# Kernel optimization log

Measured on AMD Instinct MI355X. Metric: run time of the kernel, lower is better.

Reference implementation:

```python
import jax, jax.numpy as jnp
import numpy as np

N, E, F, H = 100000, 1600000, 512, 256


def setup_inputs() -> dict:
    key = jax.random.key(0)
    ks = jax.random.split(key, 8)
    feat = jax.random.normal(ks[0], (N, F), dtype=jnp.float32)
    src = jax.random.randint(ks[1], (E,), 0, N, dtype=jnp.int32)
    dst = jax.random.randint(ks[2], (E,), 0, N, dtype=jnp.int32)
    W1 = jax.random.normal(ks[3], (F, H), dtype=jnp.float32) * 0.05
    b1 = jnp.zeros((H,), jnp.float32)
    W2 = jax.random.normal(ks[4], (H, H), dtype=jnp.float32) * 0.05
    b2 = jnp.zeros((H,), jnp.float32)
    Wg = jax.random.normal(ks[5], (3 * H, 2 * F), dtype=jnp.float32) * 0.05
    bg = jnp.zeros((2 * F,), jnp.float32)
    eps = jax.random.normal(ks[6], (F,), dtype=jnp.float32)
    return {"feat": feat, "src": src, "dst": dst, "node_index": 1234,
            "W1": W1, "b1": b1, "W2": W2, "b2": b2, "Wg": Wg, "bg": bg, "eps": eps}


def reference(feat, src, dst, node_index, W1, b1, W2, b2, Wg, bg, eps):
    n = feat.shape[0]
    ones_e = jnp.ones(src.shape[0], feat.dtype)
    out_deg = jax.ops.segment_sum(ones_e, src, num_segments=n)
    in_deg = jax.ops.segment_sum(ones_e, dst, num_segments=n)
    # DGL GraphConv(norm='both') clamps degrees to >= 1
    norm_src = jnp.maximum(out_deg, 1.0) ** -0.5  # [N]
    norm_dst = jnp.maximum(in_deg, 1.0) ** -0.5   # [N]

    def gconv(x, W, b):
        x = (x * norm_src[:, None]) @ W                      # weight first
        agg = jax.ops.segment_sum(x[src], dst, num_segments=n)  # sparse aggregate
        return agg * norm_dst[:, None] + b

    h = jax.nn.leaky_relu(gconv(feat, W1, b1), 0.01)
    h = jax.nn.leaky_relu(gconv(h, W2, b2), 0.01)
    pooled = jnp.concatenate([h.sum(0), h.max(0), h[node_index]])  # [3H]
    fd = pooled @ Wg + bg                                          # [2F]
    in_feats = feat.shape[1]
    mu = fd[:in_feats]
    sigma = jnp.abs(fd[in_feats:])
    # Normal.sample() is non-differentiable -> stop_gradient
    feat_new = jax.lax.stop_gradient(mu + sigma * eps)
    log2pi = jnp.float32(np.log(2.0 * np.pi))
    log_prob = jnp.mean(-0.5 * ((feat_new - mu) / sigma) ** 2 - jnp.log(sigma) - 0.5 * log2pi)
    return feat_new, mu, sigma, log_prob
```

## Files before the change

kernel.cpp:

```cpp
#include <hip/hip_runtime.h>
#include <math.h>

#define F_DIM 512
#define H_DIM 256

using v8bf  = __attribute__((ext_vector_type(8))) __bf16;
using f32x4 = __attribute__((ext_vector_type(4))) float;

__device__ __forceinline__ float bf2f(unsigned short u) {
    return __uint_as_float(((unsigned int)u) << 16);
}
__device__ __forceinline__ unsigned short f2bf(float f) {
    unsigned int x = __float_as_uint(f);
    unsigned int r = x + 0x7FFFu + ((x >> 16) & 1u);
    return (unsigned short)(r >> 16);
}
__device__ __forceinline__ float fp8_dec(unsigned b) {
    unsigned em = b & 0x7Fu;
    float v = (em >= 8u) ? __uint_as_float((em + 960u) << 20)
                         : (float)em * 0.001953125f;
    return (b & 0x80u) ? -v : v;
}
__device__ __forceinline__ unsigned fp8_enc(float f) {
    unsigned bits = __float_as_uint(f);
    unsigned s = (bits >> 31) << 7;
    unsigned r = bits + 0x7FFFFu + ((bits >> 20) & 1u);
    int e = (int)((r >> 23) & 0xFF);
    unsigned em;
    if (e >= 121) em = (unsigned)(((e - 120) << 3) | ((r >> 20) & 7u));
    else          em = (unsigned)__float2int_rn(fabsf(f) * 512.0f);
    return s | em;
}

__global__ void hist_kernel(const int* __restrict__ src, const int* __restrict__ dst,
                            int E, int* degO, int* degI) {
    int stride = gridDim.x * blockDim.x;
    for (int e = blockIdx.x * blockDim.x + threadIdx.x; e < E; e += stride) {
        atomicAdd(&degO[src[e]], 1);
        atomicAdd(&degI[dst[e]], 1);
    }
}

__global__ void norm_kernel(const int* __restrict__ degO, const int* __restrict__ degI,
                            int n, float* nsrc, float* ndst) {
    int i = blockIdx.x * blockDim.x + threadIdx.x;
    if (i < n) {
        nsrc[i] = rsqrtf(fmaxf((float)degO[i], 1.0f));
        ndst[i] = rsqrtf(fmaxf((float)degI[i], 1.0f));
    }
}

__global__ void scan1_kernel(const int* __restrict__ deg, int n, int* blocksums) {
    __shared__ int sm[256];
    int b = blockIdx.x, t = threadIdx.x;
    int base = b * 1024 + t * 4;
    int s = 0;
#pragma unroll
    for (int i = 0; i < 4; i++) { int idx = base + i; if (idx < n) s += deg[idx]; }
    sm[t] = s; __syncthreads();
    for (int off = 128; off > 0; off >>= 1) {
        if (t < off) sm[t] += sm[t + off];
        __syncthreads();
    }
    if (t == 0) blocksums[b] = sm[0];
}

__global__ void scan2_kernel(const int* __restrict__ blocksums, int nb, int* blockoffs) {
    if (threadIdx.x == 0 && blockIdx.x == 0) {
        int run = 0;
        for (int i = 0; i < nb; i++) { blockoffs[i] = run; run += blocksums[i]; }
    }
}

__global__ void scan3_kernel(const int* __restrict__ deg, int n,
                             const int* __restrict__ blockoffs, int* row_start) {
    __shared__ int sm[256];
    int b = blockIdx.x, t = threadIdx.x;
    int base = b * 1024 + t * 4;
    int v[4]; int s = 0;
#pragma unroll
    for (int i = 0; i < 4; i++) {
        int idx = base + i;
        v[i] = (idx < n) ? deg[idx] : 0;
        s += v[i];
    }
    sm[t] = s; __syncthreads();
    for (int off = 1; off < 256; off <<= 1) {
        int x = sm[t];
        int y = (t >= off) ? sm[t - off] : 0;
        __syncthreads();
        sm[t] = x + y;
        __syncthreads();
    }
    int run = blockoffs[b] + sm[t] - s;
#pragma unroll
    for (int i = 0; i < 4; i++) {
        int idx = base + i;
        if (idx < n) row_start[idx] = run;
        run += v[i];
    }
}

__global__ void csr_fill_kernel(const int* __restrict__ src, const int* __restrict__ dst,
                                int E, const int* __restrict__ row_start,
                                int* cursor, int* esrc) {
    int stride = gridDim.x * blockDim.x;
    for (int e = blockIdx.x * blockDim.x + threadIdx.x; e < E; e += stride) {
        int d = dst[e];
        int pos = atomicAdd(&cursor[d], 1);
        esrc[row_start[d] + pos] = src[e];
    }
}

__global__ void wt_kernel(const float* __restrict__ W, unsigned short* __restrict__ Wt, int K) {
    int idx = blockIdx.x * 256 + threadIdx.x;
    if (idx < 256 * K) {
        int n = idx / K, k = idx - n * K;
        Wt[idx] = f2bf(W[(size_t)k * 256 + n]);
    }
}

template<int KDIM, bool A_FP32>
__global__ __launch_bounds__(256) void gemm_mfma_kernel(
    const void* __restrict__ Aptr, const float* __restrict__ scale,
    const unsigned short* __restrict__ Wt, unsigned char* __restrict__ Xout, int M) {
    __shared__ unsigned short As[64 * 40];
    __shared__ unsigned short Bs[256 * 40];

    const int tid = threadIdx.x;
    const int wv = tid >> 6, ln = tid & 63;
    const int m0 = blockIdx.x * 64;
    const int sr = tid >> 2;
    const int sc = tid & 3;

    f32x4 acc[4][4];
#pragma unroll
    for (int i = 0; i < 4; i++)
#pragma unroll
        for (int j = 0; j < 4; j++) acc[i][j] = (f32x4){0.f, 0.f, 0.f, 0.f};

    const int gr = m0 + sr;
    const bool rok = (gr < M);
    float ns = 0.0f;
    if (A_FP32 && rok) ns = scale[gr];

    for (int k0 = 0; k0 < KDIM; k0 += 32) {
        if (A_FP32) {
            const float* A = (const float*)Aptr;
            float4 va = make_float4(0, 0, 0, 0), vb = make_float4(0, 0, 0, 0);
            if (rok) {
                const float* p = A + (size_t)gr * KDIM + k0 + sc * 8;
                va = *(const float4*)p;
                vb = *(const float4*)(p + 4);
            }
            uint4 u;
            u.x = (unsigned)f2bf(va.x * ns) | ((unsigned)f2bf(va.y * ns) << 16);
            u.y = (unsigned)f2bf(va.z * ns) | ((unsigned)f2bf(va.w * ns) << 16);
            u.z = (unsigned)f2bf(vb.x * ns) | ((unsigned)f2bf(vb.y * ns) << 16);
            u.w = (unsigned)f2bf(vb.z * ns) | ((unsigned)f2bf(vb.w * ns) << 16);
            *(uint4*)&As[sr * 40 + sc * 8] = u;
        } else {
            const unsigned short* A = (const unsigned short*)Aptr;
            uint4 u = make_uint4(0, 0, 0, 0);
            if (rok) u = *(const uint4*)(A + (size_t)gr * KDIM + k0 + sc * 8);
            *(uint4*)&As[sr * 40 + sc * 8] = u;
        }
#pragma unroll
        for (int i = 0; i < 4; i++) {
            int idx = tid + i * 256;
            int n = idx >> 2, ck = idx & 3;
            uint4 w = *(const uint4*)(Wt + (size_t)n * KDIM + k0 + ck * 8);
            *(uint4*)&Bs[n * 40 + ck * 8] = w;
        }
        __syncthreads();
        const int fr = ln & 15;
        const int kg = (ln >> 4) * 8;
        v8bf af[4], bfr[4];
#pragma unroll
        for (int mr = 0; mr < 4; mr++)
            af[mr] = *(const v8bf*)&As[(mr * 16 + fr) * 40 + kg];
#pragma unroll
        for (int nr = 0; nr < 4; nr++)
            bfr[nr] = *(const v8bf*)&Bs[(wv * 64 + nr * 16 + fr) * 40 + kg];
#pragma unroll
        for (int mr = 0; mr < 4; mr++)
#pragma unroll
            for (int nr = 0; nr < 4; nr++)
                acc[mr][nr] = __builtin_amdgcn_mfma_f32_16x16x32_bf16(
                    bfr[nr], af[mr], acc[mr][nr], 0, 0, 0);
        __syncthreads();
    }
#pragma unroll
    for (int mr = 0; mr < 4; mr++) {
        int grow = m0 + mr * 16 + (ln & 15);
        if (grow < M) {
#pragma unroll
            for (int nr = 0; nr < 4; nr++) {
                unsigned u = fp8_enc(acc[mr][nr][0]) | (fp8_enc(acc[mr][nr][1]) << 8) |
                             (fp8_enc(acc[mr][nr][2]) << 16) | (fp8_enc(acc[mr][nr][3]) << 24);
                *(unsigned*)(Xout + (size_t)grow * 256 + wv * 64 + nr * 16 + (ln >> 4) * 4) = u;
            }
        }
    }
}

__global__ __launch_bounds__(256) void agg_fp8_kernel(
    const unsigned char* __restrict__ xb, const int* __restrict__ esrc,
    const int* __restrict__ row_start, const int* __restrict__ degI,
    const float* __restrict__ norm_dst, const float* __restrict__ post_scale,
    const float* __restrict__ bias, unsigned short* __restrict__ hout, int n) {
    int wave = threadIdx.x >> 6;
    int lane = threadIdx.x & 63;
    int node = blockIdx.x * 4 + wave;
    if (node >= n) return;
    int start = row_start[node];
    int cnt = degI[node];

    float a0 = 0.f, a1 = 0.f, a2 = 0.f, a3 = 0.f;
    int j = 0;
    for (; j + 4 <= cnt; j += 4) {
        int s0 = esrc[start + j + 0];
        int s1 = esrc[start + j + 1];
        int s2 = esrc[start + j + 2];
        int s3 = esrc[start + j + 3];
        unsigned v0 = *(const unsigned*)(xb + (size_t)s0 * 256 + lane * 4);
        unsigned v1 = *(const unsigned*)(xb + (size_t)s1 * 256 + lane * 4);
        unsigned v2 = *(const unsigned*)(xb + (size_t)s2 * 256 + lane * 4);
        unsigned v3 = *(const unsigned*)(xb + (size_t)s3 * 256 + lane * 4);
        a0 += fp8_dec(v0 & 255u) + fp8_dec(v1 & 255u) + fp8_dec(v2 & 255u) + fp8_dec(v3 & 255u);
        a1 += fp8_dec((v0 >> 8) & 255u) + fp8_dec((v1 >> 8) & 255u) + fp8_dec((v2 >> 8) & 255u) + fp8_dec((v3 >> 8) & 255u);
        a2 += fp8_dec((v0 >> 16) & 255u) + fp8_dec((v1 >> 16) & 255u) + fp8_dec((v2 >> 16) & 255u) + fp8_dec((v3 >> 16) & 255u);
        a3 += fp8_dec(v0 >> 24) + fp8_dec(v1 >> 24) + fp8_dec(v2 >> 24) + fp8_dec(v3 >> 24);
    }
    for (; j < cnt; j++) {
        int s = esrc[start + j];
        unsigned v = *(const unsigned*)(xb + (size_t)s * 256 + lane * 4);
        a0 += fp8_dec(v & 255u);
        a1 += fp8_dec((v >> 8) & 255u);
        a2 += fp8_dec((v >> 16) & 255u);
        a3 += fp8_dec(v >> 24);
    }
    float nd = norm_dst[node];
    float ps = post_scale ? post_scale[node] : 1.0f;
    float4 bv = *(const float4*)(bias + lane * 4);
    float r0 = a0 * nd + bv.x;
    float r1 = a1 * nd + bv.y;
    float r2 = a2 * nd + bv.z;
    float r3 = a3 * nd + bv.w;
    r0 = ((r0 >= 0.f) ? r0 : 0.01f * r0) * ps;
    r1 = ((r1 >= 0.f) ? r1 : 0.01f * r1) * ps;
    r2 = ((r2 >= 0.f) ? r2 : 0.01f * r2) * ps;
    r3 = ((r3 >= 0.f) ? r3 : 0.01f * r3) * ps;
    ushort4 o;
    o.x = f2bf(r0); o.y = f2bf(r1); o.z = f2bf(r2); o.w = f2bf(r3);
    *(ushort4*)(hout + (size_t)node * 256 + lane * 4) = o;
}

__global__ void pool_partial_kernel(const unsigned short* __restrict__ h, int n,
                                    float* psum, float* pmax) {
    int b = blockIdx.x, t = threadIdx.x;
    int r0 = b * 128;
    int r1 = min(r0 + 128, n);
    float s = 0.0f, m = -INFINITY;
    for (int r = r0; r < r1; r++) {
        float v = bf2f(h[(size_t)r * 256 + t]);
        s += v;
        m = fmaxf(m, v);
    }
    psum[(size_t)b * 256 + t] = s;
    pmax[(size_t)b * 256 + t] = m;
}

__global__ void pool_mid_kernel(const float* __restrict__ psum, const float* __restrict__ pmax,
                                int nchunks, float* psum2, float* pmax2) {
    int b = blockIdx.x;
    int t = threadIdx.x;
    float s = 0.0f, m = -INFINITY;
    for (int c = b; c < nchunks; c += 32) {
        s += psum[(size_t)c * 256 + t];
        m = fmaxf(m, pmax[(size_t)c * 256 + t]);
    }
    psum2[(size_t)b * 256 + t] = s;
    pmax2[(size_t)b * 256 + t] = m;
}

__global__ void pool_final_kernel(const float* __restrict__ psum2, const float* __restrict__ pmax2,
                                  const unsigned short* __restrict__ h,
                                  const int* __restrict__ node_index, float* pooled) {
    int t = threadIdx.x;
    float s = 0.0f, m = -INFINITY;
#pragma unroll
    for (int c = 0; c < 32; c++) {
        s += psum2[(size_t)c * 256 + t];
        m = fmaxf(m, pmax2[(size_t)c * 256 + t]);
    }
    pooled[t] = s;
    pooled[256 + t] = m;
    pooled[512 + t] = bf2f(h[(size_t)(*node_index) * 256 + t]);
}

__global__ void head_gemm_kernel(const float* __restrict__ pooled,
                                 const float* __restrict__ Wg, float* fdp) {
    __shared__ float p[96];
    int t = threadIdx.x;
    int cb = blockIdx.x;
    int kb = blockIdx.y;
    if (t < 96) p[t] = pooled[kb * 96 + t];
    __syncthreads();
    int j = cb * 128 + t;
    float s = 0.0f;
#pragma unroll 8
    for (int i = 0; i < 96; i++) s += p[i] * Wg[(size_t)(kb * 96 + i) * 1024 + j];
    fdp[(size_t)kb * 1024 + j] = s;
}

__global__ void head_final_kernel(const float* __restrict__ fdp, const float* __restrict__ bg,
                                  const float* __restrict__ eps, float* __restrict__ out) {
    __shared__ float red[512];
    int t = threadIdx.x;
    float mu = bg[t];
    float sgr = bg[512 + t];
#pragma unroll
    for (int kb = 0; kb < 8; kb++) {
        mu  += fdp[(size_t)kb * 1024 + t];
        sgr += fdp[(size_t)kb * 1024 + 512 + t];
    }
    float sg = fabsf(sgr);
    float fn = mu + sg * eps[t];
    out[t] = fn;
    out[512 + t] = mu;
    out[1024 + t] = sg;
    float z = (fn - mu) / sg;
    const float LOG2PI = 1.8378770664093453f;
    float lp = -0.5f * z * z - logf(sg) - 0.5f * LOG2PI;
    red[t] = lp;
    __syncthreads();
    for (int off = 256; off > 0; off >>= 1) {
        if (t < off) red[t] += red[t + off];
        __syncthreads();
    }
    if (t == 0) out[1536] = red[0] / 512.0f;
}

extern "C" void kernel_launch(void* const* d_in, const int* in_sizes, int n_in,
                              void* d_out, int out_size, void* d_ws, size_t ws_size,
                              hipStream_t stream) {
    const float* feat = (const float*)d_in[0];
    const int* src    = (const int*)d_in[1];
    const int* dst    = (const int*)d_in[2];
    const int* nodeix = (const int*)d_in[3];
    const float* W1   = (const float*)d_in[4];
    const float* b1   = (const float*)d_in[5];
    const float* W2   = (const float*)d_in[6];
    const float* b2   = (const float*)d_in[7];
    const float* Wg   = (const float*)d_in[8];
    const float* bg   = (const float*)d_in[9];
    const float* eps  = (const float*)d_in[10];
    float* out = (float*)d_out;

    const int N = in_sizes[0] / F_DIM;
    const int E = in_sizes[1];

    char* ws = (char*)d_ws;
    size_t off = 0;
    auto alloc = [&](size_t bytes) -> char* {
        char* p = ws + off;
        off += (bytes + 511) & ~(size_t)511;
        return p;
    };
    int* degO      = (int*)alloc((size_t)N * 4);
    int* degI      = (int*)alloc((size_t)N * 4);
    float* nsrc    = (float*)alloc((size_t)N * 4);
    float* ndst    = (float*)alloc((size_t)N * 4);
    int* row_start = (int*)alloc((size_t)N * 4);
    int* cursor    = (int*)alloc((size_t)N * 4);
    int* blocksums = (int*)alloc(1024);
    int* blockoffs = (int*)alloc(1024);
    int* esrc      = (int*)alloc((size_t)E * 4);
    unsigned short* Wt1 = (unsigned short*)alloc((size_t)256 * F_DIM * 2);
    unsigned short* Wt2 = (unsigned short*)alloc((size_t)256 * H_DIM * 2);
    unsigned char* xbuf = (unsigned char*)alloc((size_t)N * H_DIM);
    unsigned short* hs  = (unsigned short*)alloc((size_t)N * H_DIM * 2);
    int nchunks = (N + 127) / 128;
    float* psum    = (float*)alloc((size_t)nchunks * 256 * 4);
    float* pmax    = (float*)alloc((size_t)nchunks * 256 * 4);
    float* psum2   = (float*)alloc((size_t)32 * 256 * 4);
    float* pmax2   = (float*)alloc((size_t)32 * 256 * 4);
    float* pooled  = (float*)alloc(768 * 4);
    float* fdp     = (float*)alloc((size_t)8 * 1024 * 4);

    hipMemsetAsync(degO, 0, (size_t)N * 4, stream);
    hipMemsetAsync(degI, 0, (size_t)N * 4, stream);
    hipMemsetAsync(cursor, 0, (size_t)N * 4, stream);

    hist_kernel<<<2048, 256, 0, stream>>>(src, dst, E, degO, degI);
    norm_kernel<<<(N + 255) / 256, 256, 0, stream>>>(degO, degI, N, nsrc, ndst);
    int nb = (N + 1023) / 1024;
    scan1_kernel<<<nb, 256, 0, stream>>>(degI, N, blocksums);
    scan2_kernel<<<1, 1, 0, stream>>>(blocksums, nb, blockoffs);
    scan3_kernel<<<nb, 256, 0, stream>>>(degI, N, blockoffs, row_start);
    csr_fill_kernel<<<2048, 256, 0, stream>>>(src, dst, E, row_start, cursor, esrc);

    wt_kernel<<<(256 * F_DIM + 255) / 256, 256, 0, stream>>>(W1, Wt1, F_DIM);
    wt_kernel<<<(256 * H_DIM + 255) / 256, 256, 0, stream>>>(W2, Wt2, H_DIM);

    int mblocks = (N + 63) / 64;
    gemm_mfma_kernel<F_DIM, true><<<mblocks, 256, 0, stream>>>(feat, nsrc, Wt1, xbuf, N);
    agg_fp8_kernel<<<(N + 3) / 4, 256, 0, stream>>>(xbuf, esrc, row_start, degI, ndst, nsrc, b1, hs, N);
    gemm_mfma_kernel<H_DIM, false><<<mblocks, 256, 0, stream>>>(hs, nullptr, Wt2, xbuf, N);
    agg_fp8_kernel<<<(N + 3) / 4, 256, 0, stream>>>(xbuf, esrc, row_start, degI, ndst, nullptr, b2, hs, N);
    pool_partial_kernel<<<nchunks, 256, 0, stream>>>(hs, N, psum, pmax);
    pool_mid_kernel<<<32, 256, 0, stream>>>(psum, pmax, nchunks, psum2, pmax2);
    pool_final_kernel<<<1, 256, 0, stream>>>(psum2, pmax2, hs, nodeix, pooled);
    head_gemm_kernel<<<dim3(8, 8), 128, 0, stream>>>(pooled, Wg, fdp);
    head_final_kernel<<<1, 512, 0, stream>>>(fdp, bg, eps, out);
}
```

Baseline: 924.8 us.

## Build CSR via two-level bucket partition with shared-memory atomics

Replaces the global-atomic degree histogram, three-kernel scan and atomic CSR fill with a bucketed counting sort. Edges are first partitioned into 512-node buckets using block-local shared counters, then each bucket builds its own degrees, row offsets and sorted edge list in shared memory. This targets the cost of scattered global atomics on node-level counters. In exchange it adds two E-sized scratch arrays and an extra pass over the edges, and it relies on node ids fitting in 17 bits and at most 200 buckets.

```diff
diff --git a/kernel.cpp b/kernel.cpp
--- a/kernel.cpp
+++ b/kernel.cpp
@@ -3,6 +3,8 @@
 
 #define F_DIM 512
 #define H_DIM 256
+#define NPB 512
+#define NBMAX 200
 
 using v8bf  = __attribute__((ext_vector_type(8))) __bf16;
 using f32x4 = __attribute__((ext_vector_type(4))) float;
@@ -32,12 +34,123 @@
     return s | em;
 }
 
-__global__ void hist_kernel(const int* __restrict__ src, const int* __restrict__ dst,
-                            int E, int* degO, int* degI) {
+__global__ __launch_bounds__(256) void bucket_count_kernel(
+    const int* __restrict__ src, const int* __restrict__ dst, int E, int nb,
+    int* bcntS, int* bcntD) {
+    __shared__ int cs[NBMAX], cd[NBMAX];
+    for (int i = threadIdx.x; i < nb; i += 256) { cs[i] = 0; cd[i] = 0; }
+    __syncthreads();
     int stride = gridDim.x * blockDim.x;
     for (int e = blockIdx.x * blockDim.x + threadIdx.x; e < E; e += stride) {
-        atomicAdd(&degO[src[e]], 1);
-        atomicAdd(&degI[dst[e]], 1);
+        atomicAdd(&cs[src[e] >> 9], 1);
+        atomicAdd(&cd[dst[e] >> 9], 1);
+    }
+    __syncthreads();
+    for (int i = threadIdx.x; i < nb; i += 256) {
+        if (cs[i]) atomicAdd(&bcntS[i], cs[i]);
+        if (cd[i]) atomicAdd(&bcntD[i], cd[i]);
+    }
+}
+
+__global__ void bucket_scan_kernel(const int* __restrict__ bcntS, const int* __restrict__ bcntD,
+                                   int nb, int* bbaseS, int* bbaseD, int* bcurS, int* bcurD) {
+    __shared__ int s1[256], s2[256];
+    int t = threadIdx.x;
+    int v1 = (t < nb) ? bcntS[t] : 0;
+    int v2 = (t < nb) ? bcntD[t] : 0;
+    s1[t] = v1; s2[t] = v2;
+    __syncthreads();
+    for (int off = 1; off < 256; off <<= 1) {
+        int a = s1[t], b = s2[t];
+        int a2 = (t >= off) ? s1[t - off] : 0;
+        int b2 = (t >= off) ? s2[t - off] : 0;
+        __syncthreads();
+        s1[t] = a + a2; s2[t] = b + b2;
+        __syncthreads();
+    }
+    if (t < nb) {
+        int eS = s1[t] - v1;
+        int eD = s2[t] - v2;
+        bbaseS[t] = eS; bbaseD[t] = eD;
+        bcurS[t] = eS;  bcurD[t] = eD;
+    }
+}
+
+__global__ __launch_bounds__(256) void partition_kernel(
+    const int* __restrict__ src, const int* __restrict__ dst, int E, int chunk, int nb,
+    int* bcurS, int* bcurD, int* __restrict__ psrc, unsigned* __restrict__ pdst) {
+    __shared__ int cs[NBMAX], cd[NBMAX], ws[NBMAX], wd[NBMAX];
+    int t = threadIdx.x;
+    for (int i = t; i < nb; i += 256) { cs[i] = 0; cd[i] = 0; }
+    __syncthreads();
+    int e0 = blockIdx.x * chunk, e1 = min(e0 + chunk, E);
+    for (int e = e0 + t; e < e1; e += 256) {
+        atomicAdd(&cs[src[e] >> 9], 1);
+        atomicAdd(&cd[dst[e] >> 9], 1);
+    }
+    __syncthreads();
+    for (int i = t; i < nb; i += 256) {
+        ws[i] = cs[i] ? atomicAdd(&bcurS[i], cs[i]) : 0;
+        wd[i] = cd[i] ? atomicAdd(&bcurD[i], cd[i]) : 0;
+    }
+    __syncthreads();
+    for (int e = e0 + t; e < e1; e += 256) {
+        int s = src[e], d = dst[e];
+        int pS = atomicAdd(&ws[s >> 9], 1);
+        psrc[pS] = s;
+        int pD = atomicAdd(&wd[d >> 9], 1);
+        pdst[pD] = (unsigned)s | ((unsigned)(d & (NPB - 1)) << 17);
+    }
+}
+
+__global__ __launch_bounds__(256) void bucket_csr_kernel(
+    const unsigned* __restrict__ pdst, const int* __restrict__ psrc,
+    const int* __restrict__ bbaseS, const int* __restrict__ bcntS,
+    const int* __restrict__ bbaseD, const int* __restrict__ bcntD,
+    int* __restrict__ degO, int* __restrict__ degI,
+    int* __restrict__ row_start, int* __restrict__ esrc, int n) {
+    __shared__ int deg[NPB];
+    __shared__ int cur[NPB];
+    __shared__ int ps[256];
+    int b = blockIdx.x, t = threadIdx.x;
+    int nbase = b << 9;
+    for (int i = t; i < NPB; i += 256) deg[i] = 0;
+    __syncthreads();
+    int eb = bbaseD[b], ec = bcntD[b];
+    for (int i = t; i < ec; i += 256) atomicAdd(&deg[pdst[eb + i] >> 17], 1);
+    __syncthreads();
+    int d0 = deg[2 * t], d1 = deg[2 * t + 1];
+    ps[t] = d0 + d1;
+    __syncthreads();
+    for (int off = 1; off < 256; off <<= 1) {
+        int v = ps[t];
+        int u = (t >= off) ? ps[t - off] : 0;
+        __syncthreads();
+        ps[t] = v + u;
+        __syncthreads();
+    }
+    int ep = ps[t] - (d0 + d1);
+    int n0 = nbase + 2 * t, n1 = nbase + 2 * t + 1;
+    if (n0 < n) { degI[n0] = d0; row_start[n0] = eb + ep; }
+    if (n1 < n) { degI[n1] = d1; row_start[n1] = eb + ep + d0; }
+    cur[2 * t] = ep;
+    cur[2 * t + 1] = ep + d0;
+    __syncthreads();
+    for (int i = t; i < ec; i += 256) {
+        unsigned v = pdst[eb + i];
+        int l = v >> 17;
+        int p = atomicAdd(&cur[l], 1);
+        esrc[eb + p] = (int)(v & 0x1FFFFu);
+    }
+    __syncthreads();
+    for (int i = t; i < NPB; i += 256) deg[i] = 0;
+    __syncthreads();
+    int sb = bbaseS[b], sc = bcntS[b];
+    for (int i = t; i < sc; i += 256) atomicAdd(&deg[psrc[sb + i] & (NPB - 1)], 1);
+    __syncthreads();
+    for (int i = t; i < NPB; i += 256) {
+        int g = nbase + i;
+        if (g < n) degO[g] = deg[i];
     }
 }
 
@@ -47,68 +160,6 @@
     if (i < n) {
         nsrc[i] = rsqrtf(fmaxf((float)degO[i], 1.0f));
         ndst[i] = rsqrtf(fmaxf((float)degI[i], 1.0f));
-    }
-}
-
-__global__ void scan1_kernel(const int* __restrict__ deg, int n, int* blocksums) {
-    __shared__ int sm[256];
-    int b = blockIdx.x, t = threadIdx.x;
-    int base = b * 1024 + t * 4;
-    int s = 0;
-#pragma unroll
-    for (int i = 0; i < 4; i++) { int idx = base + i; if (idx < n) s += deg[idx]; }
-    sm[t] = s; __syncthreads();
-    for (int off = 128; off > 0; off >>= 1) {
-        if (t < off) sm[t] += sm[t + off];
-        __syncthreads();
-    }
-    if (t == 0) blocksums[b] = sm[0];
-}
-
-__global__ void scan2_kernel(const int* __restrict__ blocksums, int nb, int* blockoffs) {
-    if (threadIdx.x == 0 && blockIdx.x == 0) {
-        int run = 0;
-        for (int i = 0; i < nb; i++) { blockoffs[i] = run; run += blocksums[i]; }
-    }
-}
-
-__global__ void scan3_kernel(const int* __restrict__ deg, int n,
-                             const int* __restrict__ blockoffs, int* row_start) {
-    __shared__ int sm[256];
-    int b = blockIdx.x, t = threadIdx.x;
-    int base = b * 1024 + t * 4;
-    int v[4]; int s = 0;
-#pragma unroll
-    for (int i = 0; i < 4; i++) {
-        int idx = base + i;
-        v[i] = (idx < n) ? deg[idx] : 0;
-        s += v[i];
-    }
-    sm[t] = s; __syncthreads();
-    for (int off = 1; off < 256; off <<= 1) {
-        int x = sm[t];
-        int y = (t >= off) ? sm[t - off] : 0;
-        __syncthreads();
-        sm[t] = x + y;
-        __syncthreads();
-    }
-    int run = blockoffs[b] + sm[t] - s;
-#pragma unroll
-    for (int i = 0; i < 4; i++) {
-        int idx = base + i;
-        if (idx < n) row_start[idx] = run;
-        run += v[i];
-    }
-}
-
-__global__ void csr_fill_kernel(const int* __restrict__ src, const int* __restrict__ dst,
-                                int E, const int* __restrict__ row_start,
-                                int* cursor, int* esrc) {
-    int stride = gridDim.x * blockDim.x;
-    for (int e = blockIdx.x * blockDim.x + threadIdx.x; e < E; e += stride) {
-        int d = dst[e];
-        int pos = atomicAdd(&cursor[d], 1);
-        esrc[row_start[d] + pos] = src[e];
     }
 }
 
@@ -360,6 +411,7 @@
 
     const int N = in_sizes[0] / F_DIM;
     const int E = in_sizes[1];
+    const int nb = (N + NPB - 1) / NPB;
 
     char* ws = (char*)d_ws;
     size_t off = 0;
@@ -373,9 +425,14 @@
     float* nsrc    = (float*)alloc((size_t)N * 4);
     float* ndst    = (float*)alloc((size_t)N * 4);
     int* row_start = (int*)alloc((size_t)N * 4);
-    int* cursor    = (int*)alloc((size_t)N * 4);
-    int* blocksums = (int*)alloc(1024);
-    int* blockoffs = (int*)alloc(1024);
+    int* bcntS     = (int*)alloc(NBMAX * 4);
+    int* bcntD     = (int*)alloc(NBMAX * 4);
+    int* bbaseS    = (int*)alloc(NBMAX * 4);
+    int* bbaseD    = (int*)alloc(NBMAX * 4);
+    int* bcurS     = (int*)alloc(NBMAX * 4);
+    int* bcurD     = (int*)alloc(NBMAX * 4);
+    int* psrc      = (int*)alloc((size_t)E * 4);
+    unsigned* pdst = (unsigned*)alloc((size_t)E * 4);
     int* esrc      = (int*)alloc((size_t)E * 4);
     unsigned short* Wt1 = (unsigned short*)alloc((size_t)256 * F_DIM * 2);
     unsigned short* Wt2 = (unsigned short*)alloc((size_t)256 * H_DIM * 2);
@@ -389,17 +446,16 @@
     float* pooled  = (float*)alloc(768 * 4);
     float* fdp     = (float*)alloc((size_t)8 * 1024 * 4);
 
-    hipMemsetAsync(degO, 0, (size_t)N * 4, stream);
-    hipMemsetAsync(degI, 0, (size_t)N * 4, stream);
-    hipMemsetAsync(cursor, 0, (size_t)N * 4, stream);
-
-    hist_kernel<<<2048, 256, 0, stream>>>(src, dst, E, degO, degI);
+    hipMemsetAsync(bcntS, 0, NBMAX * 4, stream);
+    hipMemsetAsync(bcntD, 0, NBMAX * 4, stream);
+
+    bucket_count_kernel<<<1024, 256, 0, stream>>>(src, dst, E, nb, bcntS, bcntD);
+    bucket_scan_kernel<<<1, 256, 0, stream>>>(bcntS, bcntD, nb, bbaseS, bbaseD, bcurS, bcurD);
+    int chunk = (E + 255) / 256;
+    partition_kernel<<<256, 256, 0, stream>>>(src, dst, E, chunk, nb, bcurS, bcurD, psrc, pdst);
+    bucket_csr_kernel<<<nb, 256, 0, stream>>>(pdst, psrc, bbaseS, bcntS, bbaseD, bcntD,
+                                              degO, degI, row_start, esrc, N);
     norm_kernel<<<(N + 255) / 256, 256, 0, stream>>>(degO, degI, N, nsrc, ndst);
-    int nb = (N + 1023) / 1024;
-    scan1_kernel<<<nb, 256, 0, stream>>>(degI, N, blocksums);
-    scan2_kernel<<<1, 1, 0, stream>>>(blocksums, nb, blockoffs);
-    scan3_kernel<<<nb, 256, 0, stream>>>(degI, N, blockoffs, row_start);
-    csr_fill_kernel<<<2048, 256, 0, stream>>>(src, dst, E, row_start, cursor, esrc);
 
     wt_kernel<<<(256 * F_DIM + 255) / 256, 256, 0, stream>>>(W1, Wt1, F_DIM);
     wt_kernel<<<(256 * H_DIM + 255) / 256, 256, 0, stream>>>(W2, Wt2, H_DIM);
```

Result: faster. 759.4 us (-17.9%).
